# Optimization experiments

Measured on AMD Instinct MI355X. Metric: run time of the kernel, lower is better.

The kernel has to match this reference:

```python
import jax, jax.numpy as jnp
import numpy as np

H, HD = 4, 32      # num_heads, head_dim
EPS = 1e-6         # flax LayerNorm default epsilon


def _ln(x, s, b):
    mu = jnp.mean(x, -1, keepdims=True)
    var = jnp.var(x, -1, keepdims=True)
    return (x - mu) * jax.lax.rsqrt(var + EPS) * s + b


def _pos_enc(T, D, dtype):
    # standard sinusoidal time-series positional encoding
    pos = jnp.arange(T, dtype=jnp.float32)[:, None]
    div = jnp.exp(-jnp.log(10000.0) * jnp.arange(0, D, 2, dtype=jnp.float32) / D)
    ang = pos * div
    pe = jnp.zeros((T, D), jnp.float32).at[:, 0::2].set(jnp.sin(ang)).at[:, 1::2].set(jnp.cos(ang))
    return pe.astype(dtype)


def _transformer(x, Wi, bi, Wqkv, bqkv, Wo, bo, l1s, l1b, l2s, l2b, W1, b1, W2, b2):
    # x: [B, T, in_dim] -> [B, T, D]; pre-LN transformer block with pos-enc
    B, T, _ = x.shape
    x = x @ Wi + bi
    D = x.shape[-1]
    x = x + _pos_enc(T, D, x.dtype)
    h = _ln(x, l1s, l1b)
    qkv = (h @ Wqkv + bqkv).reshape(B, T, 3, H, HD)
    q, k, v = qkv[:, :, 0], qkv[:, :, 1], qkv[:, :, 2]
    s = jnp.einsum('bthd,bshd->bhts', q, k) * (1.0 / np.sqrt(HD))
    o = jnp.einsum('bhts,bshd->bthd', jax.nn.softmax(s, -1), v).reshape(B, T, H * HD)
    x = x + (o @ Wo + bo)
    h = _ln(x, l2s, l2b)
    return x + jax.nn.gelu(h @ W1 + b1) @ W2 + b2


def _grand(h, Win, bin_, Wqk, bqk, Wout, bout, t_grid):
    # GRAND-style attention diffusion across node axis: dz/dt = (A(z) - I) z,
    # explicit Euler on the given time grid. h: [B, T, N, D]
    B, T, N, D = h.shape
    z = h @ Win + bin_
    dts = t_grid[1:] - t_grid[:-1]
    scale = 1.0 / np.sqrt(HD)
    for i in range(int(dts.shape[0])):
        qk = (z @ Wqk + bqk).reshape(B, T, N, 2, H, HD)
        q, k = qk[:, :, :, 0], qk[:, :, :, 1]
        s = jnp.einsum('btnhd,btmhd->bthnm', q, k) * scale
        A = jax.nn.softmax(s, -1).mean(axis=2)  # head-averaged [B, T, N, N]
        z = z + dts[i] * (jnp.einsum('btnm,btmd->btnd', A, z) - z)
    return z @ Wout + bout


def _forward(x, tt_Wi, tt_bi, tt_Wqkv, tt_bqkv, tt_Wo, tt_bo, tt_ln1s, tt_ln1b,
             tt_ln2s, tt_ln2b, tt_W1, tt_b1, tt_W2, tt_b2,
             g_Win, g_bin, g_Wqk, g_bqk, g_Wout, g_bout,
             ln_s, ln_b, mW1, mb1, mW2, mb2):
    # per-channel temporal transformer: vmap over node axis 2, params axis 0
    tmodel = jax.vmap(_transformer, in_axes=(2,) + (0,) * 14, out_axes=2)
    h = tmodel(x, tt_Wi, tt_bi, tt_Wqkv, tt_bqkv, tt_Wo, tt_bo,
               tt_ln1s, tt_ln1b, tt_ln2s, tt_ln2b, tt_W1, tt_b1, tt_W2, tt_b2)
    t_grid = jnp.linspace(0.0, 0.5, 4)
    h = _grand(h, g_Win, g_bin, g_Wqk, g_bqk, g_Wout, g_bout, t_grid)
    h2 = _ln(h, ln_s, ln_b)
    return jax.nn.gelu(h2 @ mW1 + mb1) @ mW2 + mb2


def setup_inputs() -> dict:
    key = jax.random.key(0)
    ks = iter(jax.random.split(key, 32))
    B, T, N, IN, D = 8, 128, 64, 32, 128
    w = lambda shape: jax.random.normal(next(ks), shape, jnp.float32) * 0.02
    z = lambda shape: jnp.zeros(shape, jnp.float32)
    o = lambda shape: jnp.ones(shape, jnp.float32)
    return dict(
        x=jax.random.normal(next(ks), (B, T, N, IN), jnp.float32),
        tt_Wi=w((N, IN, D)), tt_bi=z((N, D)),
        tt_Wqkv=w((N, D, 3 * H * HD)), tt_bqkv=z((N, 3 * H * HD)),
        tt_Wo=w((N, H * HD, D)), tt_bo=z((N, D)),
        tt_ln1s=o((N, D)), tt_ln1b=z((N, D)),
        tt_ln2s=o((N, D)), tt_ln2b=z((N, D)),
        tt_W1=w((N, D, D)), tt_b1=z((N, D)),
        tt_W2=w((N, D, D)), tt_b2=z((N, D)),
        g_Win=w((D, D)), g_bin=z((D,)),
        g_Wqk=w((D, 2 * H * HD)), g_bqk=z((2 * H * HD,)),
        g_Wout=w((D, D)), g_bout=z((D,)),
        ln_s=o((D,)), ln_b=z((D,)),
        mW1=w((D, D)), mb1=z((D,)),
        mW2=w((D, D)), mb2=z((D,)),
    )


def reference(x, tt_Wi, tt_bi, tt_Wqkv, tt_bqkv, tt_Wo, tt_bo, tt_ln1s, tt_ln1b,
              tt_ln2s, tt_ln2b, tt_W1, tt_b1, tt_W2, tt_b2,
              g_Win, g_bin, g_Wqk, g_bqk, g_Wout, g_bout,
              ln_s, ln_b, mW1, mb1, mW2, mb2):
    return _forward(x, tt_Wi, tt_bi, tt_Wqkv, tt_bqkv, tt_Wo, tt_bo, tt_ln1s, tt_ln1b,
                    tt_ln2s, tt_ln2b, tt_W1, tt_b1, tt_W2, tt_b2,
                    g_Win, g_bin, g_Wqk, g_bqk, g_Wout, g_bout,
                    ln_s, ln_b, mW1, mb1, mW2, mb2)
```

## Files before the change

kernel.cpp:

```cpp
#include <hip/hip_runtime.h>
#include <hip/hip_bf16.h>

using bf16 = __hip_bfloat16;
typedef __attribute__((ext_vector_type(8))) short short8;
typedef __attribute__((ext_vector_type(4))) float f32x4;


__device__ __forceinline__ bool isbf(const void* p) {
    return *(const unsigned*)p == 0x3F803F80u;
}
template <bool BF>
__device__ __forceinline__ float ldT(const void* p, size_t i) {
    if constexpr (BF) return __bfloat162float(((const bf16*)p)[i]);
    else              return ((const float*)p)[i];
}
template <bool BF>
__device__ __forceinline__ void stT(void* p, size_t i, float v) {
    if constexpr (BF) ((bf16*)p)[i] = __float2bfloat16(v);
    else              ((float*)p)[i] = v;
}
template <bool BF>
__device__ __forceinline__ unsigned ldbits(const void* p, size_t i) {
    if constexpr (BF) return ((const unsigned short*)p)[i];
    else {
        union { bf16 h; unsigned short u; } c;
        c.h = __float2bfloat16(((const float*)p)[i]);
        return c.u;
    }
}
__device__ __forceinline__ float b2f(bf16 x) { return __bfloat162float(x); }
__device__ __forceinline__ bf16  f2b(float x) { return __float2bfloat16(x); }
__device__ __forceinline__ unsigned short f2bu(float x) {
    union { bf16 h; unsigned short u; } c; c.h = f2b(x); return c.u;
}
__device__ __forceinline__ float bu2f(unsigned short u) {
    union { bf16 h; unsigned short u; } c; c.u = u; return b2f(c.h);
}
template <bool BF>
__device__ __forceinline__ float2 ld2T(const void* p, size_t i) {
    if constexpr (BF) {
        unsigned u = *(const unsigned*)((const unsigned short*)p + i);
        return make_float2(bu2f((unsigned short)(u & 0xffff)),
                           bu2f((unsigned short)(u >> 16)));
    } else {
        return *(const float2*)((const float*)p + i);
    }
}
__device__ __forceinline__ short8 u4_to_s8(uint4 u) {
    union { uint4 u; short8 s; } c; c.u = u; return c.s;
}
__device__ __forceinline__ unsigned pack2(float a, float b) {
    return (unsigned)f2bu(a) | ((unsigned)f2bu(b) << 16);
}
__device__ __forceinline__ float gelu_f(float x) {
    float t = fmaf(x * x * x, 0.0713548162f, 1.5957691216f * x);
    return x / (1.0f + __expf(-t));
}

template <bool BF>
__device__ __forceinline__ void ln_afrags(
    const float* __restrict__ rp, const void* __restrict__ lnsP,
    const void* __restrict__ lnbP, size_t pb, int lg, short8 af[4])
{
    float e[4][8];
    float sum = 0.f, sq = 0.f;
#pragma unroll
    for (int kk = 0; kk < 4; ++kk) {
        float4 fa = *(const float4*)(rp + 32 * kk + 8 * lg);
        float4 fb = *(const float4*)(rp + 32 * kk + 8 * lg + 4);
        e[kk][0] = fa.x; e[kk][1] = fa.y; e[kk][2] = fa.z; e[kk][3] = fa.w;
        e[kk][4] = fb.x; e[kk][5] = fb.y; e[kk][6] = fb.z; e[kk][7] = fb.w;
#pragma unroll
        for (int j = 0; j < 8; ++j) {
            sum += e[kk][j];
            sq  += e[kk][j] * e[kk][j];
        }
    }
    sum += __shfl_xor(sum, 16); sum += __shfl_xor(sum, 32);
    sq  += __shfl_xor(sq, 16);  sq  += __shfl_xor(sq, 32);
    float mu = sum * (1.0f / 128.0f);
    float var = sq * (1.0f / 128.0f) - mu * mu;
    float rs = rsqrtf(var + 1e-6f);
#pragma unroll
    for (int kk = 0; kk < 4; ++kk) {
        unsigned dw[4];
#pragma unroll
        for (int p = 0; p < 4; ++p) {
            int col = 32 * kk + 8 * lg + 2 * p;
            float2 sv = ld2T<BF>(lnsP, pb + col);
            float2 bv = ld2T<BF>(lnbP, pb + col);
            dw[p] = pack2((e[kk][2 * p]     - mu) * rs * sv.x + bv.x,
                          (e[kk][2 * p + 1] - mu) * rs * sv.y + bv.y);
        }
        af[kk] = u4_to_s8(make_uint4(dw[0], dw[1], dw[2], dw[3]));
    }
}

struct PrepArgs {
    const void* W[10];
    uint4* Wf[10];
    float* pe;
};
__device__ __constant__ const int prep_KK[10]    = {4,4,4,4,4,4,4,4,4,1};
__device__ __constant__ const int prep_NT[10]    = {24,8,8,8,8,16,8,8,8,8};
__device__ __constant__ const int prep_start[11] =
    {0,6144,8192,10240,12288,12320,12384,12416,12448,12480,12992};

template <bool BF>
__device__ __forceinline__ void prep_body(PrepArgs a) {
    int bid = blockIdx.x;
    int l = threadIdx.x;
    if (bid >= 12992) {
        int t = bid - 12992;
        int d = l * 2;
        float div0 = expf(-9.210340371976184f * (float)(d & ~1) * (1.0f / 128.0f));
        float ang = (float)t * div0;
        *(float2*)(a.pe + t * 128 + d) = make_float2(sinf(ang), cosf(ang));
        return;
    }
    int seg = 0;
#pragma unroll
    for (int s = 1; s < 10; ++s) seg += (bid >= prep_start[s]);
    int local = bid - prep_start[seg];
    int KK = prep_KK[seg], NT = prep_NT[seg];
    int kk = local % KK;
    int nt = (local / KK) % NT;
    int node = local / (KK * NT);
    int Nout = NT * 16;
    int lg = l >> 4, li = l & 15;
    int col = nt * 16 + li;
    int k0 = kk * 32 + lg * 8;
    size_t base = (size_t)node * (KK * 32) * Nout;
    const void* W = a.W[seg];
    unsigned w[4];
#pragma unroll
    for (int p = 0; p < 4; ++p) {
        unsigned lo = ldbits<BF>(W, base + (size_t)(k0 + 2 * p) * Nout + col);
        unsigned hi = ldbits<BF>(W, base + (size_t)(k0 + 2 * p + 1) * Nout + col);
        w[p] = lo | (hi << 16);
    }
    a.Wf[seg][(((size_t)node * NT + nt) * KK + kk) * 64 + l] =
        make_uint4(w[0], w[1], w[2], w[3]);
}
__global__ __launch_bounds__(64) void k_prep(PrepArgs a, const void* probe) {
    if (isbf(probe)) prep_body<true>(a);
    else             prep_body<false>(a);
}

template <bool ADD, bool PERM, bool BF>
__device__ __forceinline__ void mgemm_body(
    const uint4* __restrict__ A, const uint4* __restrict__ Wf,
    const void* __restrict__ Bias, const float* __restrict__ AddF,
    float* __restrict__ OutF, int Nout, int NT, int nodeW, int nodeB)
{
    int n64 = blockIdx.y, node = blockIdx.z;
    int row_base = blockIdx.z * 1024 + blockIdx.x * 64;
    int l = threadIdx.x, lg = l >> 4, li = l & 15;
    int wnode = nodeW ? node : 0;

    short8 bfrag[4][4];
    const uint4* wp = Wf + (((size_t)wnode * NT + n64 * 4) * 4) * 64 + l;
#pragma unroll
    for (int nt = 0; nt < 4; ++nt)
#pragma unroll
        for (int kk = 0; kk < 4; ++kk)
            bfrag[nt][kk] = u4_to_s8(wp[(nt * 4 + kk) * 64]);

    float bias[4];
#pragma unroll
    for (int nt = 0; nt < 4; ++nt)
        bias[nt] = ldT<BF>(Bias, (size_t)(nodeB ? node : 0) * Nout +
                                     n64 * 64 + nt * 16 + li);

#pragma unroll
    for (int m4 = 0; m4 < 4; ++m4) {
        int arow = row_base + m4 * 16 + li;
        short8 af[4];
        const uint4* ap = A + (size_t)arow * 16;
#pragma unroll
        for (int kk = 0; kk < 4; ++kk) af[kk] = u4_to_s8(ap[kk * 4 + lg]);
        f32x4 acc[4];
#pragma unroll
        for (int nt = 0; nt < 4; ++nt) {
            acc[nt] = (f32x4){0.f, 0.f, 0.f, 0.f};
#pragma unroll
            for (int kk = 0; kk < 4; ++kk)
                acc[nt] = __builtin_amdgcn_mfma_f32_16x16x32_bf16(
                    af[kk], bfrag[nt][kk], acc[nt], 0, 0, 0);
        }
#pragma unroll
        for (int nt = 0; nt < 4; ++nt) {
            int j = n64 * 64 + nt * 16 + li;
#pragma unroll
            for (int s = 0; s < 4; ++s) {
                int orow = row_base + m4 * 16 + (lg << 2) + s;
                int r_out = PERM ? ((orow & 1023) * 64 + (orow >> 10)) : orow;
                size_t oi = (size_t)r_out * Nout + j;
                float v = acc[nt][s] + bias[nt];
                if constexpr (ADD) v += AddF[oi];
                OutF[oi] = v;
            }
        }
    }
}
template <bool ADD, bool PERM>
__global__ __launch_bounds__(64) void k_mgemm(
    const uint4* A, const uint4* Wf, const void* Bias, const float* AddF,
    float* OutF, int Nout, int NT, int nodeW, int nodeB, const void* probe)
{
    if (isbf(probe))
        mgemm_body<ADD, PERM, true>(A, Wf, Bias, AddF, OutF, Nout, NT, nodeW, nodeB);
    else
        mgemm_body<ADD, PERM, false>(A, Wf, Bias, AddF, OutF, Nout, NT, nodeW, nodeB);
}

template <bool BF>
__device__ __forceinline__ void qkv_body(
    const float* __restrict__ X, const void* __restrict__ l1s,
    const void* __restrict__ l1b, const uint4* __restrict__ Wf,
    const void* __restrict__ Bias, unsigned short* __restrict__ Out)
{
    int tile16 = blockIdx.x, node = blockIdx.z;
    int l = threadIdx.x, lg = l >> 4, li = l & 15;
    int q = tile16 * 16 + li;

    short8 af[4];
    ln_afrags<BF>(X + ((size_t)q * 64 + node) * 128, l1s, l1b,
                  (size_t)node * 128, lg, af);
#pragma unroll
    for (int ct = 0; ct < 6; ++ct) {
#pragma unroll
        for (int nt = 0; nt < 4; ++nt) {
            short8 bfr[4];
#pragma unroll
            for (int kk = 0; kk < 4; ++kk)
                bfr[kk] = u4_to_s8(Wf[(((size_t)node * 24 + ct * 4 + nt) * 4 + kk) * 64 + l]);
            float bias = ldT<BF>(Bias, (size_t)node * 384 + ct * 64 + nt * 16 + li);
            f32x4 acc = (f32x4){0.f, 0.f, 0.f, 0.f};
#pragma unroll
            for (int kk = 0; kk < 4; ++kk)
                acc = __builtin_amdgcn_mfma_f32_16x16x32_bf16(
                    af[kk], bfr[kk], acc, 0, 0, 0);
            int j = ct * 64 + nt * 16 + li;
#pragma unroll
            for (int s = 0; s < 4; ++s) {
                int orow = node * 1024 + tile16 * 16 + (lg << 2) + s;
                Out[(size_t)orow * 384 + j] = f2bu(acc[s] + bias);
            }
        }
    }
}
__global__ __launch_bounds__(64) void k_qkv(
    const float* X, const void* l1s, const void* l1b, const uint4* Wf,
    const void* Bias, unsigned short* Out, const void* probe)
{
    if (isbf(probe)) qkv_body<true>(X, l1s, l1b, Wf, Bias, Out);
    else             qkv_body<false>(X, l1s, l1b, Wf, Bias, Out);
}

template <bool BF>
__device__ __forceinline__ void ffn_body(
    float* __restrict__ X, const void* __restrict__ l2s,
    const void* __restrict__ l2b, const uint4* __restrict__ W1f,
    const void* __restrict__ b1, const uint4* __restrict__ W2f,
    const void* __restrict__ b2, const uint4* __restrict__ Ginf,
    const void* __restrict__ gbin, unsigned short* __restrict__ Hs,
    unsigned short* __restrict__ Rs)
{
    int tile = blockIdx.x, node = blockIdx.z;
    int tid = threadIdx.x;
    int w = tid >> 6;
    int l = tid & 63, lg = l >> 4, li = l & 15;

#pragma unroll
    for (int m4 = 0; m4 < 4; ++m4) {
        int q = tile * 64 + m4 * 16 + li;
        short8 af[4];
        ln_afrags<BF>(X + ((size_t)q * 64 + node) * 128, l2s, l2b,
                      (size_t)node * 128, lg, af);
#pragma unroll
        for (int t2 = 0; t2 < 2; ++t2) {
            int nt = 2 * w + t2;
            short8 bfr[4];
#pragma unroll
            for (int kk = 0; kk < 4; ++kk)
                bfr[kk] = u4_to_s8(W1f[(((size_t)node * 8 + nt) * 4 + kk) * 64 + l]);
            float bias = ldT<BF>(b1, (size_t)node * 128 + nt * 16 + li);
            f32x4 acc = (f32x4){0.f, 0.f, 0.f, 0.f};
#pragma unroll
            for (int kk = 0; kk < 4; ++kk)
                acc = __builtin_amdgcn_mfma_f32_16x16x32_bf16(
                    af[kk], bfr[kk], acc, 0, 0, 0);
            int j = nt * 16 + li;
#pragma unroll
            for (int s = 0; s < 4; ++s) {
                int row = m4 * 16 + (lg << 2) + s;
                Hs[row * 128 + (j ^ ((row & 7) << 3))] =
                    f2bu(gelu_f(acc[s] + bias));
            }
        }
    }
    __syncthreads();
#pragma unroll
    for (int m4 = 0; m4 < 4; ++m4) {
        short8 af[4];
#pragma unroll
        for (int kk = 0; kk < 4; ++kk)
            af[kk] = u4_to_s8(*(const uint4*)&Hs[(16 * m4 + li) * 128 +
                             ((32 * kk + 8 * lg) ^ ((li & 7) << 3))]);
#pragma unroll
        for (int t2 = 0; t2 < 2; ++t2) {
            int nt = 2 * w + t2;
            short8 bfr[4];
#pragma unroll
            for (int kk = 0; kk < 4; ++kk)
                bfr[kk] = u4_to_s8(W2f[(((size_t)node * 8 + nt) * 4 + kk) * 64 + l]);
            float bias = ldT<BF>(b2, (size_t)node * 128 + nt * 16 + li);
            f32x4 acc = (f32x4){0.f, 0.f, 0.f, 0.f};
#pragma unroll
            for (int kk = 0; kk < 4; ++kk)
                acc = __builtin_amdgcn_mfma_f32_16x16x32_bf16(
                    af[kk], bfr[kk], acc, 0, 0, 0);
            int j = nt * 16 + li;
#pragma unroll
            for (int s = 0; s < 4; ++s) {
                int row = m4 * 16 + (lg << 2) + s;
                int q = tile * 64 + row;
                float v = acc[s] + bias + X[((size_t)q * 64 + node) * 128 + j];
                Rs[row * 128 + (j ^ ((row & 7) << 3))] = f2bu(v);
            }
        }
    }
    __syncthreads();
#pragma unroll
    for (int m4 = 0; m4 < 4; ++m4) {
        short8 af[4];
#pragma unroll
        for (int kk = 0; kk < 4; ++kk)
            af[kk] = u4_to_s8(*(const uint4*)&Rs[(16 * m4 + li) * 128 +
                             ((32 * kk + 8 * lg) ^ ((li & 7) << 3))]);
#pragma unroll
        for (int t2 = 0; t2 < 2; ++t2) {
            int nt = 2 * w + t2;
            short8 bfr[4];
#pragma unroll
            for (int kk = 0; kk < 4; ++kk)
                bfr[kk] = u4_to_s8(Ginf[((size_t)nt * 4 + kk) * 64 + l]);
            float bias = ldT<BF>(gbin, nt * 16 + li);
            f32x4 acc = (f32x4){0.f, 0.f, 0.f, 0.f};
#pragma unroll
            for (int kk = 0; kk < 4; ++kk)
                acc = __builtin_amdgcn_mfma_f32_16x16x32_bf16(
                    af[kk], bfr[kk], acc, 0, 0, 0);
            int j = nt * 16 + li;
#pragma unroll
            for (int s = 0; s < 4; ++s) {
                int row = m4 * 16 + (lg << 2) + s;
                int q = tile * 64 + row;
                X[((size_t)q * 64 + node) * 128 + j] = acc[s] + bias;
            }
        }
    }
}
__global__ __launch_bounds__(256) void k_ffn(
    float* X, const void* l2s, const void* l2b, const uint4* W1f,
    const void* b1, const uint4* W2f, const void* b2, const uint4* Ginf,
    const void* gbin, const void* probe)
{
    __shared__ unsigned short Hs[64 * 128];
    __shared__ unsigned short Rs[64 * 128];
    if (isbf(probe)) ffn_body<true>(X, l2s, l2b, W1f, b1, W2f, b2, Ginf, gbin, Hs, Rs);
    else             ffn_body<false>(X, l2s, l2b, W1f, b1, W2f, b2, Ginf, gbin, Hs, Rs);
}

template <bool BF>
__device__ __forceinline__ void head_body(
    const float* __restrict__ X, const void* __restrict__ lns,
    const void* __restrict__ lnb, const uint4* __restrict__ M1f,
    const void* __restrict__ mb1, const uint4* __restrict__ M2f,
    const void* __restrict__ mb2, void* __restrict__ Out,
    unsigned short* __restrict__ Hs)
{
    int row_base = blockIdx.x * 64;
    int tid = threadIdx.x;
    int w = tid >> 6;
    int l = tid & 63, lg = l >> 4, li = l & 15;

#pragma unroll
    for (int m4 = 0; m4 < 4; ++m4) {
        int arow = row_base + m4 * 16 + li;
        short8 af[4];
        ln_afrags<BF>(X + (size_t)arow * 128, lns, lnb, 0, lg, af);
#pragma unroll
        for (int t2 = 0; t2 < 2; ++t2) {
            int nt = 2 * w + t2;
            short8 bfr[4];
#pragma unroll
            for (int kk = 0; kk < 4; ++kk)
                bfr[kk] = u4_to_s8(M1f[((size_t)nt * 4 + kk) * 64 + l]);
            float bias = ldT<BF>(mb1, nt * 16 + li);
            f32x4 acc = (f32x4){0.f, 0.f, 0.f, 0.f};
#pragma unroll
            for (int kk = 0; kk < 4; ++kk)
                acc = __builtin_amdgcn_mfma_f32_16x16x32_bf16(
                    af[kk], bfr[kk], acc, 0, 0, 0);
            int j = nt * 16 + li;
#pragma unroll
            for (int s = 0; s < 4; ++s) {
                int row = m4 * 16 + (lg << 2) + s;
                Hs[row * 128 + (j ^ ((row & 7) << 3))] =
                    f2bu(gelu_f(acc[s] + bias));
            }
        }
    }
    __syncthreads();
#pragma unroll
    for (int m4 = 0; m4 < 4; ++m4) {
        short8 af[4];
#pragma unroll
        for (int kk = 0; kk < 4; ++kk)
            af[kk] = u4_to_s8(*(const uint4*)&Hs[(16 * m4 + li) * 128 +
                             ((32 * kk + 8 * lg) ^ ((li & 7) << 3))]);
#pragma unroll
        for (int t2 = 0; t2 < 2; ++t2) {
            int nt = 2 * w + t2;
            short8 bfr[4];
#pragma unroll
            for (int kk = 0; kk < 4; ++kk)
                bfr[kk] = u4_to_s8(M2f[((size_t)nt * 4 + kk) * 64 + l]);
            float bias = ldT<BF>(mb2, nt * 16 + li);
            f32x4 acc = (f32x4){0.f, 0.f, 0.f, 0.f};
#pragma unroll
            for (int kk = 0; kk < 4; ++kk)
                acc = __builtin_amdgcn_mfma_f32_16x16x32_bf16(
                    af[kk], bfr[kk], acc, 0, 0, 0);
            int j = nt * 16 + li;
#pragma unroll
            for (int s = 0; s < 4; ++s) {
                int orow = row_base + m4 * 16 + (lg << 2) + s;
                stT<BF>(Out, (size_t)orow * 128 + j, acc[s] + bias);
            }
        }
    }
}
__global__ __launch_bounds__(256) void k_head(
    const float* X, const void* lns, const void* lnb, const uint4* M1f,
    const void* mb1, const uint4* M2f, const void* mb2, void* Out,
    const void* probe)
{
    __shared__ unsigned short Hs[64 * 128];
    if (isbf(probe)) head_body<true>(X, lns, lnb, M1f, mb1, M2f, mb2, Out, Hs);
    else             head_body<false>(X, lns, lnb, M1f, mb1, M2f, mb2, Out, Hs);
}

template <bool BF>
__device__ __forceinline__ void inproj_mfma_body(
    const void* __restrict__ x, const uint4* __restrict__ WfWi,
    const void* __restrict__ bi, const float* __restrict__ pe,
    float* __restrict__ X)
{
    int tile = blockIdx.x, n64 = blockIdx.y, node = blockIdx.z;
    int l = threadIdx.x, lg = l >> 4, li = l & 15;

    short8 bfrag[4];
    float bias[4];
#pragma unroll
    for (int nt = 0; nt < 4; ++nt) {
        bfrag[nt] = u4_to_s8(WfWi[((size_t)node * 8 + n64 * 4 + nt) * 64 + l]);
        bias[nt] = ldT<BF>(bi, (size_t)node * 128 + n64 * 64 + nt * 16 + li);
    }

#pragma unroll
    for (int mt = 0; mt < 4; ++mt) {
        int q = tile * 64 + mt * 16 + li;
        size_t xoff = ((size_t)q * 64 + node) * 32 + 8 * lg;
        short8 af;
        if constexpr (BF) {
            af = u4_to_s8(*(const uint4*)((const unsigned short*)x + xoff));
        } else {
            float4 fa = *(const float4*)((const float*)x + xoff);
            float4 fb = *(const float4*)((const float*)x + xoff + 4);
            af = u4_to_s8(make_uint4(pack2(fa.x, fa.y), pack2(fa.z, fa.w),
                                     pack2(fb.x, fb.y), pack2(fb.z, fb.w)));
        }
        f32x4 acc[4];
#pragma unroll
        for (int nt = 0; nt < 4; ++nt)
            acc[nt] = __builtin_amdgcn_mfma_f32_16x16x32_bf16(
                af, bfrag[nt], (f32x4){0.f, 0.f, 0.f, 0.f}, 0, 0, 0);
#pragma unroll
        for (int nt = 0; nt < 4; ++nt) {
            int j = n64 * 64 + nt * 16 + li;
#pragma unroll
            for (int s = 0; s < 4; ++s) {
                int qo = tile * 64 + mt * 16 + (lg << 2) + s;
                size_t oi = ((size_t)qo * 64 + node) * 128 + j;
                X[oi] = acc[nt][s] + bias[nt] + pe[(qo & 127) * 128 + j];
            }
        }
    }
}
__global__ __launch_bounds__(64) void k_inproj_mfma(
    const void* x, const uint4* WfWi, const void* bi, const float* pe,
    float* X, const void* probe)
{
    if (isbf(probe)) inproj_mfma_body<true>(x, WfWi, bi, pe, X);
    else             inproj_mfma_body<false>(x, WfWi, bi, pe, X);
}

__global__ __launch_bounds__(128, 2) void k_attn(
    const unsigned short* __restrict__ QKV, bf16* __restrict__ O)
{
    int bid = blockIdx.x;
    int h = bid & 3;
    int b = (bid >> 2) & 7;
    int n = bid >> 5;
    int l = threadIdx.x & 63;
    int wv = threadIdx.x >> 6;
    int lg = l >> 4, li = l & 15;
    const float scale = 0.17677669529663687f;

    size_t panel = ((size_t)n * 1024 + b * 128) * 384;

    short8 kf[8];
#pragma unroll
    for (int kt = 0; kt < 8; ++kt) {
        const uint4* p = (const uint4*)(QKV + panel + (size_t)(kt * 16 + li) * 384
                                        + 128 + h * 32 + 8 * lg);
        kf[kt] = u4_to_s8(*p);
    }
    short8 vf[2][4];
#pragma unroll
    for (int dt = 0; dt < 2; ++dt)
#pragma unroll
        for (int kc = 0; kc < 4; ++kc) {
            unsigned dw[4];
#pragma unroll
            for (int p = 0; p < 4; ++p) {
                int t0 = kc * 32 + 8 * lg + 2 * p;
                unsigned u0 = QKV[panel + (size_t)t0 * 384 + 256 + h * 32 + dt * 16 + li];
                unsigned u1 = QKV[panel + (size_t)(t0 + 1) * 384 + 256 + h * 32 + dt * 16 + li];
                dw[p] = u0 | (u1 << 16);
            }
            vf[dt][kc] = u4_to_s8(make_uint4(dw[0], dw[1], dw[2], dw[3]));
        }

#pragma unroll
    for (int ss = 0; ss < 4; ++ss) {
        int st = wv * 4 + ss;
        const uint4* qp = (const uint4*)(QKV + panel + (size_t)(st * 16 + li) * 384
                                         + h * 32 + 8 * lg);
        short8 qf = u4_to_s8(*qp);

        f32x4 sa[8];
#pragma unroll
        for (int kt = 0; kt < 8; ++kt)
            sa[kt] = __builtin_amdgcn_mfma_f32_16x16x32_bf16(
                kf[kt], qf, (f32x4){0.f, 0.f, 0.f, 0.f}, 0, 0, 0);

        float m = -1e30f;
#pragma unroll
        for (int kt = 0; kt < 8; ++kt)
#pragma unroll
            for (int s = 0; s < 4; ++s) {
                sa[kt][s] *= scale;
                m = fmaxf(m, sa[kt][s]);
            }
        m = fmaxf(m, __shfl_xor(m, 16));
        m = fmaxf(m, __shfl_xor(m, 32));
        float lsum = 0.f;
#pragma unroll
        for (int kt = 0; kt < 8; ++kt)
#pragma unroll
            for (int s = 0; s < 4; ++s) {
                float e = __expf(sa[kt][s] - m);
                sa[kt][s] = e;
                lsum += e;
            }
        lsum += __shfl_xor(lsum, 16);
        lsum += __shfl_xor(lsum, 32);

        unsigned pdw[8][2];
#pragma unroll
        for (int kt = 0; kt < 8; ++kt) {
            pdw[kt][0] = pack2(sa[kt][0], sa[kt][1]);
            pdw[kt][1] = pack2(sa[kt][2], sa[kt][3]);
        }

        f32x4 o0 = (f32x4){0.f, 0.f, 0.f, 0.f};
        f32x4 o1 = (f32x4){0.f, 0.f, 0.f, 0.f};
#pragma unroll
        for (int kc = 0; kc < 4; ++kc) {
            unsigned bd[4];
#pragma unroll
            for (int j = 0; j < 4; ++j) {
                int src = (2 * (lg & 1) + (j >> 1)) * 16 + li;
                unsigned v0 = (unsigned)__shfl((int)pdw[2 * kc][j & 1], src);
                unsigned v1 = (unsigned)__shfl((int)pdw[2 * kc + 1][j & 1], src);
                bd[j] = (lg & 2) ? v1 : v0;
            }
            short8 pf = u4_to_s8(make_uint4(bd[0], bd[1], bd[2], bd[3]));
            o0 = __builtin_amdgcn_mfma_f32_16x16x32_bf16(vf[0][kc], pf, o0, 0, 0, 0);
            o1 = __builtin_amdgcn_mfma_f32_16x16x32_bf16(vf[1][kc], pf, o1, 0, 0, 0);
        }
        float linv = 1.0f / lsum;
        size_t obase = ((size_t)n * 1024 + b * 128 + st * 16 + li) * 128 + h * 32;
        uint2 w0, w1;
        w0.x = pack2(o0[0] * linv, o0[1] * linv);
        w0.y = pack2(o0[2] * linv, o0[3] * linv);
        w1.x = pack2(o1[0] * linv, o1[1] * linv);
        w1.y = pack2(o1[2] * linv, o1[3] * linv);
        *(uint2*)((unsigned short*)O + obase + 4 * lg)      = w0;
        *(uint2*)((unsigned short*)O + obase + 16 + 4 * lg) = w1;
    }
}

template <bool BF>
__device__ __forceinline__ void grand_fused_body(
    float* __restrict__ Xf, const uint4* __restrict__ Wqk,
    const void* __restrict__ bqk, const uint4* __restrict__ Goutf,
    const void* __restrict__ gbout,
    unsigned short* __restrict__ Zb, unsigned short* __restrict__ QKs)
{
    int bt = blockIdx.x;
    int tid = threadIdx.x;
    int w = tid >> 6;
    int h = w >> 1, wh = w & 1;
    int l = tid & 63, lg = l >> 4, li = l & 15;
    const float scale = 0.17677669529663687f;
    const float dtv = 0.16666667f;
    const int dcol = 16 * w + li;

    float zreg[4][4];
#pragma unroll
    for (int nt = 0; nt < 4; ++nt)
#pragma unroll
        for (int s = 0; s < 4; ++s) {
            int n = 16 * nt + 4 * lg + s;
            float z = Xf[((size_t)bt * 64 + n) * 128 + dcol];
            zreg[nt][s] = z;
            Zb[n * 128 + (dcol ^ ((n & 7) << 3))] = f2bu(z);
        }
    float bias[2];
#pragma unroll
    for (int jt = 0; jt < 2; ++jt)
        bias[jt] = ldT<BF>(bqk, 32 * w + 16 * jt + li);
    __syncthreads();

    for (int it = 0; it < 3; ++it) {
#pragma unroll
        for (int jt = 0; jt < 2; ++jt) {
            short8 bfr[4];
#pragma unroll
            for (int kk = 0; kk < 4; ++kk)
                bfr[kk] = u4_to_s8(Wqk[(((2 * w + jt) * 4) + kk) * 64 + l]);
#pragma unroll
            for (int mt = 0; mt < 4; ++mt) {
                short8 af[4];
#pragma unroll
                for (int kk = 0; kk < 4; ++kk)
                    af[kk] = u4_to_s8(*(const uint4*)&Zb[(16 * mt + li) * 128 +
                                     ((32 * kk + 8 * lg) ^ ((li & 7) << 3))]);
                f32x4 acc = (f32x4){0.f, 0.f, 0.f, 0.f};
#pragma unroll
                for (int kk = 0; kk < 4; ++kk)
                    acc = __builtin_amdgcn_mfma_f32_16x16x32_bf16(
                        af[kk], bfr[kk], acc, 0, 0, 0);
#pragma unroll
                for (int s = 0; s < 4; ++s) {
                    int row = 16 * mt + 4 * lg + s;
                    QKs[row * 256 + ((32 * w + 16 * jt + li) ^ ((row & 7) << 3))] =
                        f2bu(acc[s] + bias[jt]);
                }
            }
        }
        __syncthreads();
        short8 kf[4], qf[2];
#pragma unroll
        for (int kt = 0; kt < 4; ++kt)
            kf[kt] = u4_to_s8(*(const uint4*)&QKs[(16 * kt + li) * 256 +
                              ((128 + 32 * h + 8 * lg) ^ ((li & 7) << 3))]);
#pragma unroll
        for (int j = 0; j < 2; ++j)
            qf[j] = u4_to_s8(*(const uint4*)&QKs[(16 * (2 * wh + j) + li) * 256 +
                             ((32 * h + 8 * lg) ^ ((li & 7) << 3))]);
        __syncthreads();

        f32x4 sa[4][2];
#pragma unroll
        for (int kt = 0; kt < 4; ++kt)
#pragma unroll
            for (int j = 0; j < 2; ++j)
                sa[kt][j] = __builtin_amdgcn_mfma_f32_16x16x32_bf16(
                    kf[kt], qf[j], (f32x4){0.f, 0.f, 0.f, 0.f}, 0, 0, 0);
        float mx[2], sm[2];
#pragma unroll
        for (int j = 0; j < 2; ++j) mx[j] = -1e30f;
#pragma unroll
        for (int kt = 0; kt < 4; ++kt)
#pragma unroll
            for (int j = 0; j < 2; ++j)
#pragma unroll
                for (int s = 0; s < 4; ++s) {
                    sa[kt][j][s] *= scale;
                    mx[j] = fmaxf(mx[j], sa[kt][j][s]);
                }
#pragma unroll
        for (int j = 0; j < 2; ++j) {
            mx[j] = fmaxf(mx[j], __shfl_xor(mx[j], 16));
            mx[j] = fmaxf(mx[j], __shfl_xor(mx[j], 32));
            sm[j] = 0.f;
        }
#pragma unroll
        for (int kt = 0; kt < 4; ++kt)
#pragma unroll
            for (int j = 0; j < 2; ++j)
#pragma unroll
                for (int s = 0; s < 4; ++s) {
                    float e = __expf(sa[kt][j][s] - mx[j]);
                    sa[kt][j][s] = e;
                    sm[j] += e;
                }
#pragma unroll
        for (int j = 0; j < 2; ++j) {
            sm[j] += __shfl_xor(sm[j], 16);
            sm[j] += __shfl_xor(sm[j], 32);
            sm[j] = 0.25f / sm[j];
        }
#pragma unroll
        for (int kt = 0; kt < 4; ++kt)
#pragma unroll
            for (int j = 0; j < 2; ++j) {
                int q = 16 * (2 * wh + j) + li;
                int col0 = 64 * h + 16 * kt + 4 * lg;
                int ix = q * 256 + (col0 ^ ((q & 7) << 3));
                *(unsigned*)&QKs[ix]     = pack2(sa[kt][j][0] * sm[j],
                                                 sa[kt][j][1] * sm[j]);
                *(unsigned*)&QKs[ix + 2] = pack2(sa[kt][j][2] * sm[j],
                                                 sa[kt][j][3] * sm[j]);
            }
        __syncthreads();
        unsigned pz[4][2];
#pragma unroll
        for (int nt = 0; nt < 4; ++nt) {
            pz[nt][0] = pack2(zreg[nt][0], zreg[nt][1]);
            pz[nt][1] = pack2(zreg[nt][2], zreg[nt][3]);
        }
        short8 bz[2];
#pragma unroll
        for (int kk = 0; kk < 2; ++kk) {
            unsigned dw[4];
#pragma unroll
            for (int p = 0; p < 4; ++p) {
                int src = ((2 * lg + (p >> 1)) & 3) * 16 + li;
                unsigned v0 = (unsigned)__shfl((int)pz[2 * kk][p & 1], src);
                unsigned v1 = (unsigned)__shfl((int)pz[2 * kk + 1][p & 1], src);
                dw[p] = (lg & 2) ? v1 : v0;
            }
            bz[kk] = u4_to_s8(make_uint4(dw[0], dw[1], dw[2], dw[3]));
        }
        f32x4 oz[4];
#pragma unroll
        for (int nt = 0; nt < 4; ++nt) oz[nt] = (f32x4){0.f, 0.f, 0.f, 0.f};
#pragma unroll
        for (int hh = 0; hh < 4; ++hh)
#pragma unroll
            for (int kk = 0; kk < 2; ++kk)
#pragma unroll
                for (int nt = 0; nt < 4; ++nt) {
                    short8 af = u4_to_s8(*(const uint4*)&QKs[(16 * nt + li) * 256 +
                                 ((64 * hh + 32 * kk + 8 * lg) ^ ((li & 7) << 3))]);
                    oz[nt] = __builtin_amdgcn_mfma_f32_16x16x32_bf16(
                        af, bz[kk], oz[nt], 0, 0, 0);
                }
#pragma unroll
        for (int nt = 0; nt < 4; ++nt)
#pragma unroll
            for (int s = 0; s < 4; ++s) {
                int n = 16 * nt + 4 * lg + s;
                float z = zreg[nt][s];
                float zn = z + dtv * (oz[nt][s] - z);
                zreg[nt][s] = zn;
                Zb[n * 128 + (dcol ^ ((n & 7) << 3))] = f2bu(zn);
            }
        __syncthreads();
    }
    {
        short8 gb[4];
#pragma unroll
        for (int kk = 0; kk < 4; ++kk)
            gb[kk] = u4_to_s8(Goutf[((size_t)w * 4 + kk) * 64 + l]);
        float gbias = ldT<BF>(gbout, 16 * w + li);
#pragma unroll
        for (int mt = 0; mt < 4; ++mt) {
            short8 af[4];
#pragma unroll
            for (int kk = 0; kk < 4; ++kk)
                af[kk] = u4_to_s8(*(const uint4*)&Zb[(16 * mt + li) * 128 +
                                 ((32 * kk + 8 * lg) ^ ((li & 7) << 3))]);
            f32x4 acc = (f32x4){0.f, 0.f, 0.f, 0.f};
#pragma unroll
            for (int kk = 0; kk < 4; ++kk)
                acc = __builtin_amdgcn_mfma_f32_16x16x32_bf16(
                    af[kk], gb[kk], acc, 0, 0, 0);
#pragma unroll
            for (int s = 0; s < 4; ++s) {
                int n = 16 * mt + 4 * lg + s;
                Xf[((size_t)bt * 64 + n) * 128 + 16 * w + li] = acc[s] + gbias;
            }
        }
    }
}
__global__ __launch_bounds__(512, 2) void k_grand_fused(
    float* Xf, const uint4* Wqk, const void* bqk, const uint4* Goutf,
    const void* gbout, const void* probe)
{
    __shared__ unsigned short Zb[64 * 128];
    __shared__ unsigned short QKs[64 * 256];
    if (isbf(probe)) grand_fused_body<true>(Xf, Wqk, bqk, Goutf, gbout, Zb, QKs);
    else             grand_fused_body<false>(Xf, Wqk, bqk, Goutf, gbout, Zb, QKs);
}

extern "C" void kernel_launch(void* const* d_in, const int* in_sizes, int n_in,
                              void* d_out, int out_size, void* d_ws, size_t ws_size,
                              hipStream_t stream)
{
    const void* x     = d_in[0];
    const void* tWi   = d_in[1];
    const void* tbi   = d_in[2];
    const void* tWqkv = d_in[3];
    const void* tbqkv = d_in[4];
    const void* tWo   = d_in[5];
    const void* tbo   = d_in[6];
    const void* l1s   = d_in[7];
    const void* l1b   = d_in[8];
    const void* l2s   = d_in[9];
    const void* l2b   = d_in[10];
    const void* tW1   = d_in[11];
    const void* tb1   = d_in[12];
    const void* tW2   = d_in[13];
    const void* tb2   = d_in[14];
    const void* gWin  = d_in[15];
    const void* gbin  = d_in[16];
    const void* gWqk  = d_in[17];
    const void* gbqk  = d_in[18];
    const void* gWout = d_in[19];
    const void* gbout = d_in[20];
    const void* lns   = d_in[21];
    const void* lnb   = d_in[22];
    const void* mW1   = d_in[23];
    const void* mb1   = d_in[24];
    const void* mW2   = d_in[25];
    const void* mb2   = d_in[26];
    const void* probe = lns;

    const size_t MiB = 1u << 20;
    char* ws = (char*)d_ws;

    float* X   = (float*)ws;
    float* pe  = (float*)(ws + 61 * MiB);
    bf16*  S16 = (bf16*)(ws + 64 * MiB);
    bf16*  bfA = (bf16*)(ws + 112 * MiB);

    char* wf = ws + 32 * MiB;
    uint4* WfQKV = (uint4*)(wf);
    uint4* WfWo  = (uint4*)(wf + 6291456);
    uint4* WfW1  = (uint4*)(wf + 8388608);
    uint4* WfW2  = (uint4*)(wf + 10485760);
    uint4* WfGin = (uint4*)(wf + 12582912);
    uint4* WfGqk = (uint4*)(wf + 12615680);
    uint4* WfGout= (uint4*)(wf + 12681216);
    uint4* WfM1  = (uint4*)(wf + 12713984);
    uint4* WfM2  = (uint4*)(wf + 12746752);
    uint4* WfWi  = (uint4*)(wf + 12779520);

    PrepArgs pa;
    pa.W[0] = tWqkv; pa.Wf[0] = WfQKV;
    pa.W[1] = tWo;   pa.Wf[1] = WfWo;
    pa.W[2] = tW1;   pa.Wf[2] = WfW1;
    pa.W[3] = tW2;   pa.Wf[3] = WfW2;
    pa.W[4] = gWin;  pa.Wf[4] = WfGin;
    pa.W[5] = gWqk;  pa.Wf[5] = WfGqk;
    pa.W[6] = gWout; pa.Wf[6] = WfGout;
    pa.W[7] = mW1;   pa.Wf[7] = WfM1;
    pa.W[8] = mW2;   pa.Wf[8] = WfM2;
    pa.W[9] = tWi;   pa.Wf[9] = WfWi;
    pa.pe = pe;
    k_prep<<<13120, 64, 0, stream>>>(pa, probe);

    k_inproj_mfma<<<dim3(16, 2, 64), 64, 0, stream>>>(x, WfWi, tbi, pe, X, probe);
    k_qkv<<<dim3(64, 1, 64), 64, 0, stream>>>(
        X, l1s, l1b, WfQKV, tbqkv, (unsigned short*)S16, probe);
    k_attn<<<2048, 128, 0, stream>>>((const unsigned short*)S16, bfA);
    k_mgemm<true, true><<<dim3(16, 2, 64), 64, 0, stream>>>(
        (const uint4*)bfA, WfWo, tbo, X, X, 128, 8, 1, 1, probe);
    k_ffn<<<dim3(16, 1, 64), 256, 0, stream>>>(
        X, l2s, l2b, WfW1, tb1, WfW2, tb2, WfGin, gbin, probe);

    k_grand_fused<<<1024, 512, 0, stream>>>(X, WfGqk, gbqk, WfGout, gbout, probe);

    k_head<<<1024, 256, 0, stream>>>(
        X, lns, lnb, WfM1, mb1, WfM2, mb2, d_out, probe);
}
```

Before: 259.9 us.

## Tile QKV over 64 rows, hoist weight fragments, stage GRAND output in LDS

The QKV kernel now handles 64 rows per block instead of 16, with a quarter as many blocks, so each weight fragment loaded from global memory is reused across four row tiles. In the FFN and head kernels, weight fragments and biases are loaded once per phase rather than once per row tile. The GRAND output projection writes its fp32 results to shared memory first and then copies them out with coalesced float4 stores instead of scattered scalar stores. The trade-offs are higher register pressure in the QKV kernel, fewer blocks to spread across the GPU, and an extra barrier in the GRAND kernel.

New measurement: 238.4 us. -8.3%, faster.

```diff
diff --git a/kernel.cpp b/kernel.cpp
--- a/kernel.cpp
+++ b/kernel.cpp
@@ -220,32 +220,46 @@
     const void* __restrict__ l1b, const uint4* __restrict__ Wf,
     const void* __restrict__ Bias, unsigned short* __restrict__ Out)
 {
-    int tile16 = blockIdx.x, node = blockIdx.z;
+    int tile = blockIdx.x, node = blockIdx.z;
     int l = threadIdx.x, lg = l >> 4, li = l & 15;
-    int q = tile16 * 16 + li;
-
-    short8 af[4];
-    ln_afrags<BF>(X + ((size_t)q * 64 + node) * 128, l1s, l1b,
-                  (size_t)node * 128, lg, af);
+
+    short8 af[4][4];
+#pragma unroll
+    for (int m4 = 0; m4 < 4; ++m4) {
+        int q = tile * 64 + m4 * 16 + li;
+        ln_afrags<BF>(X + ((size_t)q * 64 + node) * 128, l1s, l1b,
+                      (size_t)node * 128, lg, af[m4]);
+    }
 #pragma unroll
     for (int ct = 0; ct < 6; ++ct) {
+        short8 bfr[4][4];
+        float bias[4];
 #pragma unroll
         for (int nt = 0; nt < 4; ++nt) {
-            short8 bfr[4];
-#pragma unroll
-            for (int kk = 0; kk < 4; ++kk)
-                bfr[kk] = u4_to_s8(Wf[(((size_t)node * 24 + ct * 4 + nt) * 4 + kk) * 64 + l]);
-            float bias = ldT<BF>(Bias, (size_t)node * 384 + ct * 64 + nt * 16 + li);
-            f32x4 acc = (f32x4){0.f, 0.f, 0.f, 0.f};
-#pragma unroll
-            for (int kk = 0; kk < 4; ++kk)
-                acc = __builtin_amdgcn_mfma_f32_16x16x32_bf16(
-                    af[kk], bfr[kk], acc, 0, 0, 0);
-            int j = ct * 64 + nt * 16 + li;
-#pragma unroll
-            for (int s = 0; s < 4; ++s) {
-                int orow = node * 1024 + tile16 * 16 + (lg << 2) + s;
-                Out[(size_t)orow * 384 + j] = f2bu(acc[s] + bias);
+#pragma unroll
+            for (int kk = 0; kk < 4; ++kk)
+                bfr[nt][kk] = u4_to_s8(Wf[(((size_t)node * 24 + ct * 4 + nt) * 4 + kk) * 64 + l]);
+            bias[nt] = ldT<BF>(Bias, (size_t)node * 384 + ct * 64 + nt * 16 + li);
+        }
+#pragma unroll
+        for (int m4 = 0; m4 < 4; ++m4) {
+            f32x4 acc[4];
+#pragma unroll
+            for (int nt = 0; nt < 4; ++nt) {
+                acc[nt] = (f32x4){0.f, 0.f, 0.f, 0.f};
+#pragma unroll
+                for (int kk = 0; kk < 4; ++kk)
+                    acc[nt] = __builtin_amdgcn_mfma_f32_16x16x32_bf16(
+                        af[m4][kk], bfr[nt][kk], acc[nt], 0, 0, 0);
+            }
+#pragma unroll
+            for (int nt = 0; nt < 4; ++nt) {
+                int j = ct * 64 + nt * 16 + li;
+#pragma unroll
+                for (int s = 0; s < 4; ++s) {
+                    int orow = node * 1024 + tile * 64 + m4 * 16 + (lg << 2) + s;
+                    Out[(size_t)orow * 384 + j] = f2bu(acc[nt][s] + bias[nt]);
+                }
             }
         }
     }
@@ -272,92 +286,114 @@
     int w = tid >> 6;
     int l = tid & 63, lg = l >> 4, li = l & 15;
 
-#pragma unroll
-    for (int m4 = 0; m4 < 4; ++m4) {
-        int q = tile * 64 + m4 * 16 + li;
-        short8 af[4];
-        ln_afrags<BF>(X + ((size_t)q * 64 + node) * 128, l2s, l2b,
-                      (size_t)node * 128, lg, af);
+    {
+        short8 bfr[2][4];
+        float biasv[2];
 #pragma unroll
         for (int t2 = 0; t2 < 2; ++t2) {
             int nt = 2 * w + t2;
-            short8 bfr[4];
-#pragma unroll
-            for (int kk = 0; kk < 4; ++kk)
-                bfr[kk] = u4_to_s8(W1f[(((size_t)node * 8 + nt) * 4 + kk) * 64 + l]);
-            float bias = ldT<BF>(b1, (size_t)node * 128 + nt * 16 + li);
-            f32x4 acc = (f32x4){0.f, 0.f, 0.f, 0.f};
-#pragma unroll
-            for (int kk = 0; kk < 4; ++kk)
-                acc = __builtin_amdgcn_mfma_f32_16x16x32_bf16(
-                    af[kk], bfr[kk], acc, 0, 0, 0);
-            int j = nt * 16 + li;
-#pragma unroll
-            for (int s = 0; s < 4; ++s) {
-                int row = m4 * 16 + (lg << 2) + s;
-                Hs[row * 128 + (j ^ ((row & 7) << 3))] =
-                    f2bu(gelu_f(acc[s] + bias));
+#pragma unroll
+            for (int kk = 0; kk < 4; ++kk)
+                bfr[t2][kk] = u4_to_s8(W1f[(((size_t)node * 8 + nt) * 4 + kk) * 64 + l]);
+            biasv[t2] = ldT<BF>(b1, (size_t)node * 128 + nt * 16 + li);
+        }
+#pragma unroll
+        for (int m4 = 0; m4 < 4; ++m4) {
+            int q = tile * 64 + m4 * 16 + li;
+            short8 af[4];
+            ln_afrags<BF>(X + ((size_t)q * 64 + node) * 128, l2s, l2b,
+                          (size_t)node * 128, lg, af);
+#pragma unroll
+            for (int t2 = 0; t2 < 2; ++t2) {
+                int nt = 2 * w + t2;
+                f32x4 acc = (f32x4){0.f, 0.f, 0.f, 0.f};
+#pragma unroll
+                for (int kk = 0; kk < 4; ++kk)
+                    acc = __builtin_amdgcn_mfma_f32_16x16x32_bf16(
+                        af[kk], bfr[t2][kk], acc, 0, 0, 0);
+                int j = nt * 16 + li;
+#pragma unroll
+                for (int s = 0; s < 4; ++s) {
+                    int row = m4 * 16 + (lg << 2) + s;
+                    Hs[row * 128 + (j ^ ((row & 7) << 3))] =
+                        f2bu(gelu_f(acc[s] + biasv[t2]));
+                }
             }
         }
     }
     __syncthreads();
-#pragma unroll
-    for (int m4 = 0; m4 < 4; ++m4) {
-        short8 af[4];
-#pragma unroll
-        for (int kk = 0; kk < 4; ++kk)
-            af[kk] = u4_to_s8(*(const uint4*)&Hs[(16 * m4 + li) * 128 +
-                             ((32 * kk + 8 * lg) ^ ((li & 7) << 3))]);
+    {
+        short8 bfr[2][4];
+        float biasv[2];
 #pragma unroll
         for (int t2 = 0; t2 < 2; ++t2) {
             int nt = 2 * w + t2;
-            short8 bfr[4];
-#pragma unroll
-            for (int kk = 0; kk < 4; ++kk)
-                bfr[kk] = u4_to_s8(W2f[(((size_t)node * 8 + nt) * 4 + kk) * 64 + l]);
-            float bias = ldT<BF>(b2, (size_t)node * 128 + nt * 16 + li);
-            f32x4 acc = (f32x4){0.f, 0.f, 0.f, 0.f};
-#pragma unroll
-            for (int kk = 0; kk < 4; ++kk)
-                acc = __builtin_amdgcn_mfma_f32_16x16x32_bf16(
-                    af[kk], bfr[kk], acc, 0, 0, 0);
-            int j = nt * 16 + li;
-#pragma unroll
-            for (int s = 0; s < 4; ++s) {
-                int row = m4 * 16 + (lg << 2) + s;
-                int q = tile * 64 + row;
-                float v = acc[s] + bias + X[((size_t)q * 64 + node) * 128 + j];
-                Rs[row * 128 + (j ^ ((row & 7) << 3))] = f2bu(v);
+#pragma unroll
+            for (int kk = 0; kk < 4; ++kk)
+                bfr[t2][kk] = u4_to_s8(W2f[(((size_t)node * 8 + nt) * 4 + kk) * 64 + l]);
+            biasv[t2] = ldT<BF>(b2, (size_t)node * 128 + nt * 16 + li);
+        }
+#pragma unroll
+        for (int m4 = 0; m4 < 4; ++m4) {
+            short8 af[4];
+#pragma unroll
+            for (int kk = 0; kk < 4; ++kk)
+                af[kk] = u4_to_s8(*(const uint4*)&Hs[(16 * m4 + li) * 128 +
+                                 ((32 * kk + 8 * lg) ^ ((li & 7) << 3))]);
+#pragma unroll
+            for (int t2 = 0; t2 < 2; ++t2) {
+                int nt = 2 * w + t2;
+                f32x4 acc = (f32x4){0.f, 0.f, 0.f, 0.f};
+#pragma unroll
+                for (int kk = 0; kk < 4; ++kk)
+                    acc = __builtin_amdgcn_mfma_f32_16x16x32_bf16(
+                        af[kk], bfr[t2][kk], acc, 0, 0, 0);
+                int j = nt * 16 + li;
+#pragma unroll
+                for (int s = 0; s < 4; ++s) {
+                    int row = m4 * 16 + (lg << 2) + s;
+                    int q = tile * 64 + row;
+                    float v = acc[s] + biasv[t2] +
+                              X[((size_t)q * 64 + node) * 128 + j];
+                    Rs[row * 128 + (j ^ ((row & 7) << 3))] = f2bu(v);
+                }
             }
         }
     }
     __syncthreads();
-#pragma unroll
-    for (int m4 = 0; m4 < 4; ++m4) {
-        short8 af[4];
-#pragma unroll
-        for (int kk = 0; kk < 4; ++kk)
-            af[kk] = u4_to_s8(*(const uint4*)&Rs[(16 * m4 + li) * 128 +
-                             ((32 * kk + 8 * lg) ^ ((li & 7) << 3))]);
+    {
+        short8 bfr[2][4];
+        float biasv[2];
 #pragma unroll
         for (int t2 = 0; t2 < 2; ++t2) {
             int nt = 2 * w + t2;
-            short8 bfr[4];
-#pragma unroll
-            for (int kk = 0; kk < 4; ++kk)
-                bfr[kk] = u4_to_s8(Ginf[((size_t)nt * 4 + kk) * 64 + l]);
-            float bias = ldT<BF>(gbin, nt * 16 + li);
-            f32x4 acc = (f32x4){0.f, 0.f, 0.f, 0.f};
-#pragma unroll
-            for (int kk = 0; kk < 4; ++kk)
-                acc = __builtin_amdgcn_mfma_f32_16x16x32_bf16(
-                    af[kk], bfr[kk], acc, 0, 0, 0);
-            int j = nt * 16 + li;
-#pragma unroll
-            for (int s = 0; s < 4; ++s) {
-                int row = m4 * 16 + (lg << 2) + s;
-                int q = tile * 64 + row;
-                X[((size_t)q * 64 + node) * 128 + j] = acc[s] + bias;
+#pragma unroll
+            for (int kk = 0; kk < 4; ++kk)
+                bfr[t2][kk] = u4_to_s8(Ginf[((size_t)nt * 4 + kk) * 64 + l]);
+            biasv[t2] = ldT<BF>(gbin, nt * 16 + li);
+        }
+#pragma unroll
+        for (int m4 = 0; m4 < 4; ++m4) {
+            short8 af[4];
+#pragma unroll
+            for (int kk = 0; kk < 4; ++kk)
+                af[kk] = u4_to_s8(*(const uint4*)&Rs[(16 * m4 + li) * 128 +
+                                 ((32 * kk + 8 * lg) ^ ((li & 7) << 3))]);
+#pragma unroll
+            for (int t2 = 0; t2 < 2; ++t2) {
+                int nt = 2 * w + t2;
+                f32x4 acc = (f32x4){0.f, 0.f, 0.f, 0.f};
+#pragma unroll
+                for (int kk = 0; kk < 4; ++kk)
+                    acc = __builtin_amdgcn_mfma_f32_16x16x32_bf16(
+                        af[kk], bfr[t2][kk], acc, 0, 0, 0);
+                int j = nt * 16 + li;
+#pragma unroll
+                for (int s = 0; s < 4; ++s) {
+                    int row = m4 * 16 + (lg << 2) + s;
+                    int q = tile * 64 + row;
+                    X[((size_t)q * 64 + node) * 128 + j] = acc[s] + biasv[t2];
+                }
             }
         }
     }
@@ -386,59 +422,73 @@
     int w = tid >> 6;
     int l = tid & 63, lg = l >> 4, li = l & 15;
 
-#pragma unroll
-    for (int m4 = 0; m4 < 4; ++m4) {
-        int arow = row_base + m4 * 16 + li;
-        short8 af[4];
-        ln_afrags<BF>(X + (size_t)arow * 128, lns, lnb, 0, lg, af);
+    {
+        short8 bfr[2][4];
+        float biasv[2];
 #pragma unroll
         for (int t2 = 0; t2 < 2; ++t2) {
             int nt = 2 * w + t2;
-            short8 bfr[4];
-#pragma unroll
-            for (int kk = 0; kk < 4; ++kk)
-                bfr[kk] = u4_to_s8(M1f[((size_t)nt * 4 + kk) * 64 + l]);
-            float bias = ldT<BF>(mb1, nt * 16 + li);
-            f32x4 acc = (f32x4){0.f, 0.f, 0.f, 0.f};
-#pragma unroll
-            for (int kk = 0; kk < 4; ++kk)
-                acc = __builtin_amdgcn_mfma_f32_16x16x32_bf16(
-                    af[kk], bfr[kk], acc, 0, 0, 0);
-            int j = nt * 16 + li;
-#pragma unroll
-            for (int s = 0; s < 4; ++s) {
-                int row = m4 * 16 + (lg << 2) + s;
-                Hs[row * 128 + (j ^ ((row & 7) << 3))] =
-                    f2bu(gelu_f(acc[s] + bias));
+#pragma unroll
+            for (int kk = 0; kk < 4; ++kk)
+                bfr[t2][kk] = u4_to_s8(M1f[((size_t)nt * 4 + kk) * 64 + l]);
+            biasv[t2] = ldT<BF>(mb1, nt * 16 + li);
+        }
+#pragma unroll
+        for (int m4 = 0; m4 < 4; ++m4) {
+            int arow = row_base + m4 * 16 + li;
+            short8 af[4];
+            ln_afrags<BF>(X + (size_t)arow * 128, lns, lnb, 0, lg, af);
+#pragma unroll
+            for (int t2 = 0; t2 < 2; ++t2) {
+                int nt = 2 * w + t2;
+                f32x4 acc = (f32x4){0.f, 0.f, 0.f, 0.f};
+#pragma unroll
+                for (int kk = 0; kk < 4; ++kk)
+                    acc = __builtin_amdgcn_mfma_f32_16x16x32_bf16(
+                        af[kk], bfr[t2][kk], acc, 0, 0, 0);
+                int j = nt * 16 + li;
+#pragma unroll
+                for (int s = 0; s < 4; ++s) {
+                    int row = m4 * 16 + (lg << 2) + s;
+                    Hs[row * 128 + (j ^ ((row & 7) << 3))] =
+                        f2bu(gelu_f(acc[s] + biasv[t2]));
+                }
             }
         }
     }
     __syncthreads();
-#pragma unroll
-    for (int m4 = 0; m4 < 4; ++m4) {
-        short8 af[4];
-#pragma unroll
-        for (int kk = 0; kk < 4; ++kk)
-            af[kk] = u4_to_s8(*(const uint4*)&Hs[(16 * m4 + li) * 128 +
-                             ((32 * kk + 8 * lg) ^ ((li & 7) << 3))]);
+    {
+        short8 bfr[2][4];
+        float biasv[2];
 #pragma unroll
         for (int t2 = 0; t2 < 2; ++t2) {
             int nt = 2 * w + t2;
-            short8 bfr[4];
-#pragma unroll
-            for (int kk = 0; kk < 4; ++kk)
-                bfr[kk] = u4_to_s8(M2f[((size_t)nt * 4 + kk) * 64 + l]);
-            float bias = ldT<BF>(mb2, nt * 16 + li);
-            f32x4 acc = (f32x4){0.f, 0.f, 0.f, 0.f};
-#pragma unroll
-            for (int kk = 0; kk < 4; ++kk)
-                acc = __builtin_amdgcn_mfma_f32_16x16x32_bf16(
-                    af[kk], bfr[kk], acc, 0, 0, 0);
-            int j = nt * 16 + li;
-#pragma unroll
-            for (int s = 0; s < 4; ++s) {
-                int orow = row_base + m4 * 16 + (lg << 2) + s;
-                stT<BF>(Out, (size_t)orow * 128 + j, acc[s] + bias);
+#pragma unroll
+            for (int kk = 0; kk < 4; ++kk)
+                bfr[t2][kk] = u4_to_s8(M2f[((size_t)nt * 4 + kk) * 64 + l]);
+            biasv[t2] = ldT<BF>(mb2, nt * 16 + li);
+        }
+#pragma unroll
+        for (int m4 = 0; m4 < 4; ++m4) {
+            short8 af[4];
+#pragma unroll
+            for (int kk = 0; kk < 4; ++kk)
+                af[kk] = u4_to_s8(*(const uint4*)&Hs[(16 * m4 + li) * 128 +
+                                 ((32 * kk + 8 * lg) ^ ((li & 7) << 3))]);
+#pragma unroll
+            for (int t2 = 0; t2 < 2; ++t2) {
+                int nt = 2 * w + t2;
+                f32x4 acc = (f32x4){0.f, 0.f, 0.f, 0.f};
+#pragma unroll
+                for (int kk = 0; kk < 4; ++kk)
+                    acc = __builtin_amdgcn_mfma_f32_16x16x32_bf16(
+                        af[kk], bfr[t2][kk], acc, 0, 0, 0);
+                int j = nt * 16 + li;
+#pragma unroll
+                for (int s = 0; s < 4; ++s) {
+                    int orow = row_base + m4 * 16 + (lg << 2) + s;
+                    stT<BF>(Out, (size_t)orow * 128 + j, acc[s] + biasv[t2]);
+                }
             }
         }
     }
@@ -786,6 +836,7 @@
         __syncthreads();
     }
     {
+        float* QKf = (float*)QKs;
         short8 gb[4];
 #pragma unroll
         for (int kk = 0; kk < 4; ++kk)
@@ -806,8 +857,14 @@
 #pragma unroll
             for (int s = 0; s < 4; ++s) {
                 int n = 16 * mt + 4 * lg + s;
-                Xf[((size_t)bt * 64 + n) * 128 + 16 * w + li] = acc[s] + gbias;
-            }
+                QKf[n * 128 + 16 * w + li] = acc[s] + gbias;
+            }
+        }
+        __syncthreads();
+        for (int idx = tid; idx < 2048; idx += 512) {
+            int row = idx >> 5, c = idx & 31;
+            ((float4*)Xf)[((size_t)bt * 64 + row) * 32 + c] =
+                ((const float4*)QKf)[row * 32 + c];
         }
     }
 }
@@ -889,7 +946,7 @@
     k_prep<<<13120, 64, 0, stream>>>(pa, probe);
 
     k_inproj_mfma<<<dim3(16, 2, 64), 64, 0, stream>>>(x, WfWi, tbi, pe, X, probe);
-    k_qkv<<<dim3(64, 1, 64), 64, 0, stream>>>(
+    k_qkv<<<dim3(16, 1, 64), 64, 0, stream>>>(
         X, l1s, l1b, WfQKV, tbqkv, (unsigned short*)S16, probe);
     k_attn<<<2048, 128, 0, stream>>>((const unsigned short*)S16, bfA);
     k_mgemm<true, true><<<dim3(16, 2, 64), 64, 0, stream>>>(
```
